# Optimization experiments

Hardware: AMD Instinct MI355X
Metric: run time of the kernel (lower is better)

The kernel has to match this reference:

```python
import jax, jax.numpy as jnp
import numpy as np

N_NODES = 100000
N_EDGES = 3200000
IN_DIM = 128
HID_DIM = 128
N_LAYERS = 3


def setup_inputs() -> dict:
    key = jax.random.key(0)
    ks = jax.random.split(key, 3 + 2 * N_LAYERS)
    inp = {
        "feats": jax.random.normal(ks[0], (N_NODES, IN_DIM), dtype=jnp.float32),
        "edge_src": jax.random.randint(ks[1], (N_EDGES,), 0, N_NODES, dtype=jnp.int32),
        "edge_dst": jax.random.randint(ks[2], (N_EDGES,), 0, N_NODES, dtype=jnp.int32),
    }
    d_in = IN_DIM
    for l in range(N_LAYERS):
        scale = 1.0 / np.sqrt(d_in)
        inp[f"W{l}"] = jax.random.uniform(ks[3 + 2 * l], (d_in, HID_DIM), jnp.float32, -scale, scale)
        inp[f"b{l}"] = jax.random.uniform(ks[4 + 2 * l], (HID_DIM,), jnp.float32, -scale, scale)
        inp[f"eps{l}"] = jnp.zeros((), jnp.float32)  # learn_eps init 0
        d_in = HID_DIM
    return inp


def _gin_layer(h, src, dst, W, b, eps):
    # sum aggregation over in-neighbors: agg[i] = sum_{(s->i)} h[s]
    agg = jax.ops.segment_sum(h[src], dst, num_segments=N_NODES)
    return ((1.0 + eps) * h + agg) @ W + b


def reference(feats, edge_src, edge_dst, W0, b0, eps0, W1, b1, eps1, W2, b2, eps2):
    h = feats
    for W, b, eps in ((W0, b0, eps0), (W1, b1, eps1), (W2, b2, eps2)):
        h = _gin_layer(h, edge_src, edge_dst, W, b, eps)
        # dropout is identity at p=0 / eval
    return h
```

## Files before the change

### kernel.cpp

```cpp
#include <hip/hip_runtime.h>

#define N_NODES 100000
#define N_EDGES 3200000
#define DIM 128
#define GROWS (N_NODES + 1)
#define NBUCK 391
#define NBP 392
#define EB_BLOCKS 782
#define BSLACK 2048
#define MAXPAD 9984

typedef __attribute__((ext_vector_type(8))) short short8;
typedef __attribute__((ext_vector_type(4))) float f32x4;


__device__ __forceinline__ unsigned rne_bf16(float f) {
    unsigned u = __builtin_bit_cast(unsigned, f);
    return (u + 0x7FFFu + ((u >> 16) & 1u)) >> 16;
}
__device__ __forceinline__ float bf16lo(unsigned u) {
    return __builtin_bit_cast(float, u << 16);
}
__device__ __forceinline__ float bf16hi(unsigned u) {
    return __builtin_bit_cast(float, u & 0xFFFF0000u);
}
__device__ __forceinline__ void split2(float x, unsigned short& h, unsigned short& l) {
    unsigned hu = rne_bf16(x);
    h = (unsigned short)hu;
    l = (unsigned short)rne_bf16(x - bf16lo(hu));
}


__global__ __launch_bounds__(256) void bhist_k(const int* __restrict__ dst,
                                               int* __restrict__ bucketTotal,
                                               int* __restrict__ bhArr) {
    __shared__ int h[NBP];
    int tid = threadIdx.x;
    for (int i = tid; i < NBP; i += 256) h[i] = 0;
    __syncthreads();
#pragma unroll
    for (int c = 0; c < 4; c++) {
        int e = blockIdx.x * 4096 + c * 1024 + tid * 4;
        if (e < N_EDGES) {
            int4 d4 = ((const int4*)dst)[e >> 2];
            atomicAdd(&h[d4.x >> 8], 1);
            atomicAdd(&h[d4.y >> 8], 1);
            atomicAdd(&h[d4.z >> 8], 1);
            atomicAdd(&h[d4.w >> 8], 1);
        }
    }
    __syncthreads();
    for (int i = tid; i < NBP; i += 256) {
        int v = h[i];
        bhArr[blockIdx.x * NBP + i] = v;
        if (v > 0) atomicAdd(&bucketTotal[i], v);
    }
}

__global__ __launch_bounds__(512) void bscan_k(const int* __restrict__ bucketTotal,
                                               int* __restrict__ bucketBase,
                                               int* __restrict__ bucketCursor) {
    __shared__ int tmp[512];
    int tid = threadIdx.x;
    int v = (tid < NBP) ? bucketTotal[tid] : 0;
    tmp[tid] = v;
    __syncthreads();
    for (int off = 1; off < 512; off <<= 1) {
        int x = tmp[tid];
        if (tid >= off) x += tmp[tid - off];
        __syncthreads();
        tmp[tid] = x;
        __syncthreads();
    }
    if (tid < NBP) {
        int excl = tmp[tid] - v;
        bucketBase[tid] = excl;
        bucketCursor[tid] = excl;
        if (tid == NBP - 1) bucketBase[NBP] = tmp[tid];
    }
}

__global__ __launch_bounds__(512) void bscatter_k(const int* __restrict__ src,
                                                  const int* __restrict__ dst,
                                                  const int* __restrict__ bhArr,
                                                  int* __restrict__ bucketCursor,
                                                  int* __restrict__ ebuf) {
    __shared__ int lcur0[NBP];
    __shared__ int pexc[NBP];
    __shared__ int lofs[NBP];
    __shared__ int pfx[512];
    __shared__ int sortedv[4096];
    __shared__ int gaddr[4096];
    int tid = threadIdx.x;
    int bid = blockIdx.x;
    int v = 0;
    if (tid < NBP) {
        v = bhArr[bid * NBP + tid];
        lcur0[tid] = (v > 0) ? atomicAdd(&bucketCursor[tid], v) : 0;
    }
    pfx[tid] = v;
    __syncthreads();
    for (int off = 1; off < 512; off <<= 1) {
        int x = pfx[tid];
        if (tid >= off) x += pfx[tid - off];
        __syncthreads();
        pfx[tid] = x;
        __syncthreads();
    }
    if (tid < NBP) {
        int ex = pfx[tid] - v;
        pexc[tid] = ex;
        lofs[tid] = ex;
    }
    __syncthreads();
#pragma unroll
    for (int c = 0; c < 2; c++) {
        int e = bid * 4096 + c * 2048 + tid * 4;
        if (e < N_EDGES) {
            int4 d4 = ((const int4*)dst)[e >> 2];
            int4 s4 = ((const int4*)src)[e >> 2];
            int b0 = d4.x >> 8, b1 = d4.y >> 8, b2 = d4.z >> 8, b3 = d4.w >> 8;
            int t0 = atomicAdd(&lofs[b0], 1);
            int t1 = atomicAdd(&lofs[b1], 1);
            int t2 = atomicAdd(&lofs[b2], 1);
            int t3 = atomicAdd(&lofs[b3], 1);
            sortedv[t0] = (s4.x << 8) | (d4.x & 255);
            sortedv[t1] = (s4.y << 8) | (d4.y & 255);
            sortedv[t2] = (s4.z << 8) | (d4.z & 255);
            sortedv[t3] = (s4.w << 8) | (d4.w & 255);
            gaddr[t0] = lcur0[b0] + (t0 - pexc[b0]);
            gaddr[t1] = lcur0[b1] + (t1 - pexc[b1]);
            gaddr[t2] = lcur0[b2] + (t2 - pexc[b2]);
            gaddr[t3] = lcur0[b3] + (t3 - pexc[b3]);
        }
    }
    __syncthreads();
    int totalE = min(4096, N_EDGES - bid * 4096);
    for (int j = tid; j < totalE; j += 512)
        ebuf[gaddr[j]] = sortedv[j];
}

__global__ __launch_bounds__(256) void bfinal_k(const int* __restrict__ ebuf,
                                                const int* __restrict__ bucketBase,
                                                int* __restrict__ offsets,
                                                int* __restrict__ nbArr,
                                                int* __restrict__ csr) {
    __shared__ int srt[MAXPAD];
    __shared__ int cnt[256];
    __shared__ int sc[256];
    __shared__ int cur[256];
    int tid = threadIdx.x;
    int b = blockIdx.x;
    int s = bucketBase[b], e = bucketBase[b + 1];
    int m = e - s;
    cnt[tid] = 0;
    __syncthreads();
    for (int i = tid; i < m; i += 256)
        atomicAdd(&cnt[ebuf[s + i] & 255], 1);
    __syncthreads();
    int c = cnt[tid];
    int pad = (c + 3) & ~3;
    sc[tid] = pad;
    __syncthreads();
    for (int off = 1; off < 256; off <<= 1) {
        int x = sc[tid];
        if (tid >= off) x += sc[tid - off];
        __syncthreads();
        sc[tid] = x;
        __syncthreads();
    }
    int pexcl = sc[tid] - pad;
    int gbase = s + b * BSLACK;
    int node = b * 256 + tid;
    if (node < N_NODES) {
        offsets[node] = gbase + pexcl;
        nbArr[node] = pad >> 2;
    }
    cur[tid] = pexcl;
    __syncthreads();
    int padTot = sc[255];
    if (padTot <= MAXPAD) {
        for (int j = tid; j < padTot; j += 256) srt[j] = N_NODES;
        __syncthreads();
        for (int i = tid; i < m; i += 256) {
            int pk = ebuf[s + i];
            int pos = atomicAdd(&cur[pk & 255], 1);
            srt[pos] = (int)((unsigned)pk >> 8);
        }
        __syncthreads();
        for (int j = tid; j < padTot; j += 256)
            csr[gbase + j] = srt[j];
    } else {
        for (int i = tid; i < m; i += 256) {
            int pk = ebuf[s + i];
            int pos = atomicAdd(&cur[pk & 255], 1);
            csr[gbase + pos] = (int)((unsigned)pk >> 8);
        }
        __syncthreads();
        int pend = pexcl + pad;
        for (int p2 = cur[tid]; p2 < pend; p2++) csr[gbase + p2] = N_NODES;
    }
}


__global__ __launch_bounds__(64) void prepw_k(const float* __restrict__ W,
                                              unsigned short* __restrict__ Wh,
                                              unsigned short* __restrict__ Wl) {
    int l = threadIdx.x;
    int t = blockIdx.x;
    int col = ((t >> 2) << 4) + (l & 15);
    int k0 = ((t & 3) << 5) + ((l >> 4) << 3);
    unsigned hw[4], lw[4];
#pragma unroll
    for (int p = 0; p < 4; p++) {
        float x0 = W[(size_t)(k0 + 2 * p) * DIM + col];
        float x1 = W[(size_t)(k0 + 2 * p + 1) * DIM + col];
        unsigned short h0, l0, h1, l1;
        split2(x0, h0, l0);
        split2(x1, h1, l1);
        hw[p] = (unsigned)h0 | ((unsigned)h1 << 16);
        lw[p] = (unsigned)l0 | ((unsigned)l1 << 16);
    }
    size_t base = ((size_t)t * 64 + l) * 8;
    *(uint4*)(Wh + base) = make_uint4(hw[0], hw[1], hw[2], hw[3]);
    *(uint4*)(Wl + base) = make_uint4(lw[0], lw[1], lw[2], lw[3]);
}

__global__ __launch_bounds__(256) void gemm_k(const float* __restrict__ H,
                                              const unsigned short* __restrict__ Wh,
                                              const unsigned short* __restrict__ Wl,
                                              unsigned short* __restrict__ G) {
    int tid = threadIdx.x;
    int l = tid & 63;
    int wv = tid >> 6;
    int rowBase = blockIdx.x * 64 + wv * 16;
    int r = rowBase + (l & 15);
    int kg = (l >> 4) << 3;
    const float* hp = H + (size_t)((r < N_NODES) ? r : 0) * DIM;
    float zmask = (r < N_NODES) ? 1.0f : 0.0f;

    f32x4 acc[8];
#pragma unroll
    for (int cb = 0; cb < 8; cb++) acc[cb] = (f32x4){0.f, 0.f, 0.f, 0.f};

#pragma unroll
    for (int ks = 0; ks < 4; ks++) {
        float4 u0 = *(const float4*)(hp + ks * 32 + kg);
        float4 u1 = *(const float4*)(hp + ks * 32 + kg + 4);
        short8 ah, al;
        unsigned short hh, ll;
        split2(u0.x * zmask, hh, ll); ah[0] = hh; al[0] = ll;
        split2(u0.y * zmask, hh, ll); ah[1] = hh; al[1] = ll;
        split2(u0.z * zmask, hh, ll); ah[2] = hh; al[2] = ll;
        split2(u0.w * zmask, hh, ll); ah[3] = hh; al[3] = ll;
        split2(u1.x * zmask, hh, ll); ah[4] = hh; al[4] = ll;
        split2(u1.y * zmask, hh, ll); ah[5] = hh; al[5] = ll;
        split2(u1.z * zmask, hh, ll); ah[6] = hh; al[6] = ll;
        split2(u1.w * zmask, hh, ll); ah[7] = hh; al[7] = ll;
#pragma unroll
        for (int cb = 0; cb < 8; cb++) {
            size_t fidx = (size_t)((cb * 4 + ks) * 64 + l) * 8;
            short8 bh = *(const short8*)(Wh + fidx);
            short8 bl = *(const short8*)(Wl + fidx);
            acc[cb] = __builtin_amdgcn_mfma_f32_16x16x32_bf16(ah, bh, acc[cb], 0, 0, 0);
            acc[cb] = __builtin_amdgcn_mfma_f32_16x16x32_bf16(al, bh, acc[cb], 0, 0, 0);
            acc[cb] = __builtin_amdgcn_mfma_f32_16x16x32_bf16(ah, bl, acc[cb], 0, 0, 0);
        }
    }

    int ro = rowBase + ((l >> 4) << 2);
    int co = l & 15;
#pragma unroll
    for (int cb = 0; cb < 8; cb++) {
#pragma unroll
        for (int j = 0; j < 4; j++) {
            int rr = ro + j;
            if (rr <= N_NODES)
                G[(size_t)rr * DIM + cb * 16 + co] = (unsigned short)rne_bf16(acc[cb][j]);
        }
    }
}

__device__ __forceinline__ void accum8(float* acc, uint4 v) {
    acc[0] += bf16lo(v.x); acc[1] += bf16hi(v.x);
    acc[2] += bf16lo(v.y); acc[3] += bf16hi(v.y);
    acc[4] += bf16lo(v.z); acc[5] += bf16hi(v.z);
    acc[6] += bf16lo(v.w); acc[7] += bf16hi(v.w);
}

__global__ __launch_bounds__(256) void agg_k(const unsigned short* __restrict__ G,
                                             const int* __restrict__ off,
                                             const int* __restrict__ nbArr,
                                             const int* __restrict__ csr,
                                             const float* __restrict__ bias,
                                             const float* __restrict__ epsp,
                                             float* __restrict__ out) {
    int tid = threadIdx.x;
    int lane = tid & 63;
    int node = blockIdx.x * 4 + (tid >> 6);
    int quarter = lane >> 4;
    int q = lane & 15;
    float e1 = 1.0f + epsp[0];

    int offA = off[node];
    int nb = nbArr[node];
    const int* clb = csr + offA + quarter;

    float acc[8] = {0.f, 0.f, 0.f, 0.f, 0.f, 0.f, 0.f, 0.f};

    int b = 0;
    for (; b + 4 <= nb; b += 4) {
        int i0 = clb[0];
        int i1 = clb[4];
        int i2 = clb[8];
        int i3 = clb[12];
        clb += 16;
        uint4 g0 = *(const uint4*)(G + (size_t)i0 * DIM + q * 8);
        uint4 g1 = *(const uint4*)(G + (size_t)i1 * DIM + q * 8);
        uint4 g2 = *(const uint4*)(G + (size_t)i2 * DIM + q * 8);
        uint4 g3 = *(const uint4*)(G + (size_t)i3 * DIM + q * 8);
        accum8(acc, g0);
        accum8(acc, g1);
        accum8(acc, g2);
        accum8(acc, g3);
    }
    for (; b < nb; b++) {
        int i0 = clb[0];
        clb += 4;
        uint4 g0 = *(const uint4*)(G + (size_t)i0 * DIM + q * 8);
        accum8(acc, g0);
    }

#pragma unroll
    for (int j = 0; j < 8; j++) {
        acc[j] += __shfl_xor(acc[j], 16);
        acc[j] += __shfl_xor(acc[j], 32);
    }

    if (quarter == 0) {
        uint4 sv = *(const uint4*)(G + (size_t)node * DIM + q * 8);
        float4 b0 = *(const float4*)(bias + q * 8);
        float4 b1 = *(const float4*)(bias + q * 8 + 4);
        float* op = out + (size_t)node * DIM + q * 8;
        float4 r0, r1;
        r0.x = acc[0] + e1 * bf16lo(sv.x) + b0.x;
        r0.y = acc[1] + e1 * bf16hi(sv.x) + b0.y;
        r0.z = acc[2] + e1 * bf16lo(sv.y) + b0.z;
        r0.w = acc[3] + e1 * bf16hi(sv.y) + b0.w;
        r1.x = acc[4] + e1 * bf16lo(sv.z) + b1.x;
        r1.y = acc[5] + e1 * bf16hi(sv.z) + b1.y;
        r1.z = acc[6] + e1 * bf16lo(sv.w) + b1.z;
        r1.w = acc[7] + e1 * bf16hi(sv.w) + b1.w;
        *(float4*)op = r0;
        *(float4*)(op + 4) = r1;
    }
}


extern "C" void kernel_launch(void* const* d_in, const int* in_sizes, int n_in,
                              void* d_out, int out_size, void* d_ws, size_t ws_size,
                              hipStream_t stream) {
    const float* feats = (const float*)d_in[0];
    const int* esrc = (const int*)d_in[1];
    const int* edst = (const int*)d_in[2];
    const float* Wm[3] = {(const float*)d_in[3], (const float*)d_in[6], (const float*)d_in[9]};
    const float* Bv[3] = {(const float*)d_in[4], (const float*)d_in[7], (const float*)d_in[10]};
    const float* Ev[3] = {(const float*)d_in[5], (const float*)d_in[8], (const float*)d_in[11]};
    float* out = (float*)d_out;

    char* ws = (char*)d_ws;
    unsigned short* bufG = (unsigned short*)(ws);
    int* ebuf       = (int*)(ws + 25600512);
    int* csr        = (int*)(ws + 38400512);
    int* offsets    = (int*)(ws + 54411776);
    int* nbArr      = (int*)(ws + 54811776);
    int* bucketTotal= (int*)(ws + 55211776);
    int* bucketBase = (int*)(ws + 55213376);
    int* bucketCur  = (int*)(ws + 55215040);
    int* bhArr      = (int*)(ws + 55216640);
    unsigned short* wfrag = (unsigned short*)(ws + 56442816);

    for (int l = 0; l < 3; l++)
        prepw_k<<<32, 64, 0, stream>>>(Wm[l], wfrag + l * 32768, wfrag + l * 32768 + 16384);

    hipMemsetAsync(bucketTotal, 0, NBP * sizeof(int), stream);
    bhist_k<<<EB_BLOCKS, 256, 0, stream>>>(edst, bucketTotal, bhArr);
    bscan_k<<<1, 512, 0, stream>>>(bucketTotal, bucketBase, bucketCur);
    bscatter_k<<<EB_BLOCKS, 512, 0, stream>>>(esrc, edst, bhArr, bucketCur, ebuf);
    bfinal_k<<<NBUCK, 256, 0, stream>>>(ebuf, bucketBase, offsets, nbArr, csr);

    const float* h = feats;
    for (int l = 0; l < 3; l++) {
        gemm_k<<<(N_NODES + 63) / 64, 256, 0, stream>>>(h, wfrag + l * 32768,
                                                        wfrag + l * 32768 + 16384, bufG);
        agg_k<<<N_NODES / 4, 256, 0, stream>>>(bufG, offsets, nbArr, csr, Bv[l], Ev[l], out);
        h = out;
    }
}
```

Baseline: 595.6 us.

## Fuse neighbor aggregation with next layer GEMM to keep bf16 intermediates

Adds an aggemm_k kernel. It aggregates neighbor rows for 16 nodes per 1024-thread block, stages the fp32 result in shared memory, then runs the next layer's split-bf16 MFMA GEMM and writes bf16 output directly. It replaces the per-layer gemm_k plus agg_k pair for the first two layers, so the fp32 hidden states are no longer written and re-read through global memory. It also folds the three weight-prep launches into one, ping-pongs intermediates between the workspace and the output buffer, and zeroes the padding row. Only half the waves do the GEMM stage, and the large blocks with a barrier may reduce latency hiding during the gather.

```diff
diff --git a/kernel.cpp b/kernel.cpp
--- a/kernel.cpp
+++ b/kernel.cpp
@@ -203,11 +203,16 @@
 }
 
 
-__global__ __launch_bounds__(64) void prepw_k(const float* __restrict__ W,
-                                              unsigned short* __restrict__ Wh,
-                                              unsigned short* __restrict__ Wl) {
+__global__ __launch_bounds__(64) void prepw_k(const float* __restrict__ W0,
+                                              const float* __restrict__ W1,
+                                              const float* __restrict__ W2,
+                                              unsigned short* __restrict__ wfrag) {
     int l = threadIdx.x;
-    int t = blockIdx.x;
+    int lay = blockIdx.x >> 5;
+    int t = blockIdx.x & 31;
+    const float* W = (lay == 0) ? W0 : (lay == 1) ? W1 : W2;
+    unsigned short* Wh = wfrag + lay * 32768;
+    unsigned short* Wl = Wh + 16384;
     int col = ((t >> 2) << 4) + (l & 15);
     int k0 = ((t & 3) << 5) + ((l >> 4) << 3);
     unsigned hw[4], lw[4];
@@ -286,6 +291,106 @@
     acc[2] += bf16lo(v.y); acc[3] += bf16hi(v.y);
     acc[4] += bf16lo(v.z); acc[5] += bf16hi(v.z);
     acc[6] += bf16lo(v.w); acc[7] += bf16hi(v.w);
+}
+
+__global__ __launch_bounds__(1024) void aggemm_k(const unsigned short* __restrict__ G,
+                                                 const int* __restrict__ off,
+                                                 const int* __restrict__ nbArr,
+                                                 const int* __restrict__ csr,
+                                                 const float* __restrict__ bias,
+                                                 const float* __restrict__ epsp,
+                                                 const unsigned short* __restrict__ Wh,
+                                                 const unsigned short* __restrict__ Wl,
+                                                 unsigned short* __restrict__ Gout) {
+    __shared__ float hsm[16][132];
+    int tid = threadIdx.x;
+    int lane = tid & 63;
+    int wid = tid >> 6;
+    int node = blockIdx.x * 16 + wid;
+    int quarter = lane >> 4;
+    int q = lane & 15;
+    float e1 = 1.0f + epsp[0];
+
+    int offA = off[node];
+    int nb = nbArr[node];
+    const int* clb = csr + offA + quarter;
+    float acc[8] = {0.f, 0.f, 0.f, 0.f, 0.f, 0.f, 0.f, 0.f};
+    int b = 0;
+    for (; b + 4 <= nb; b += 4) {
+        int i0 = clb[0];
+        int i1 = clb[4];
+        int i2 = clb[8];
+        int i3 = clb[12];
+        clb += 16;
+        uint4 g0 = *(const uint4*)(G + (size_t)i0 * DIM + q * 8);
+        uint4 g1 = *(const uint4*)(G + (size_t)i1 * DIM + q * 8);
+        uint4 g2 = *(const uint4*)(G + (size_t)i2 * DIM + q * 8);
+        uint4 g3 = *(const uint4*)(G + (size_t)i3 * DIM + q * 8);
+        accum8(acc, g0);
+        accum8(acc, g1);
+        accum8(acc, g2);
+        accum8(acc, g3);
+    }
+    for (; b < nb; b++) {
+        int i0 = clb[0];
+        clb += 4;
+        uint4 g0 = *(const uint4*)(G + (size_t)i0 * DIM + q * 8);
+        accum8(acc, g0);
+    }
+#pragma unroll
+    for (int j = 0; j < 8; j++) {
+        acc[j] += __shfl_xor(acc[j], 16);
+        acc[j] += __shfl_xor(acc[j], 32);
+    }
+    if (quarter == 0) {
+        uint4 sv = *(const uint4*)(G + (size_t)node * DIM + q * 8);
+        float4 b0 = *(const float4*)(bias + q * 8);
+        float4 b1 = *(const float4*)(bias + q * 8 + 4);
+        float4 r0, r1;
+        r0.x = acc[0] + e1 * bf16lo(sv.x) + b0.x;
+        r0.y = acc[1] + e1 * bf16hi(sv.x) + b0.y;
+        r0.z = acc[2] + e1 * bf16lo(sv.y) + b0.z;
+        r0.w = acc[3] + e1 * bf16hi(sv.y) + b0.w;
+        r1.x = acc[4] + e1 * bf16lo(sv.z) + b1.x;
+        r1.y = acc[5] + e1 * bf16hi(sv.z) + b1.y;
+        r1.z = acc[6] + e1 * bf16lo(sv.w) + b1.z;
+        r1.w = acc[7] + e1 * bf16hi(sv.w) + b1.w;
+        *(float4*)&hsm[wid][q * 8] = r0;
+        *(float4*)&hsm[wid][q * 8 + 4] = r1;
+    }
+    __syncthreads();
+
+    if (wid < 8) {
+        int cb = wid;
+        int rl = lane & 15;
+        int kg = (lane >> 4) << 3;
+        f32x4 o = (f32x4){0.f, 0.f, 0.f, 0.f};
+#pragma unroll
+        for (int ks = 0; ks < 4; ks++) {
+            const float* ap = &hsm[rl][ks * 32 + kg];
+            short8 ah, al;
+            unsigned short hh, ll;
+#pragma unroll
+            for (int j = 0; j < 8; j++) {
+                split2(ap[j], hh, ll);
+                ah[j] = hh;
+                al[j] = ll;
+            }
+            size_t fidx = (size_t)((cb * 4 + ks) * 64 + lane) * 8;
+            short8 bh = *(const short8*)(Wh + fidx);
+            short8 bl = *(const short8*)(Wl + fidx);
+            o = __builtin_amdgcn_mfma_f32_16x16x32_bf16(ah, bh, o, 0, 0, 0);
+            o = __builtin_amdgcn_mfma_f32_16x16x32_bf16(al, bh, o, 0, 0, 0);
+            o = __builtin_amdgcn_mfma_f32_16x16x32_bf16(ah, bl, o, 0, 0, 0);
+        }
+        int ro = blockIdx.x * 16 + ((lane >> 4) << 2);
+        int co = cb * 16 + rl;
+#pragma unroll
+        for (int j = 0; j < 4; j++)
+            Gout[(size_t)(ro + j) * DIM + co] = (unsigned short)rne_bf16(o[j]);
+    } else if (wid == 8 && blockIdx.x == 0) {
+        ((unsigned*)(Gout + (size_t)N_NODES * DIM))[lane] = 0u;
+    }
 }
 
 __global__ __launch_bounds__(256) void agg_k(const unsigned short* __restrict__ G,
@@ -380,8 +485,10 @@
     int* bhArr      = (int*)(ws + 55216640);
     unsigned short* wfrag = (unsigned short*)(ws + 56442816);
 
-    for (int l = 0; l < 3; l++)
-        prepw_k<<<32, 64, 0, stream>>>(Wm[l], wfrag + l * 32768, wfrag + l * 32768 + 16384);
+    unsigned short* G_A = bufG;
+    unsigned short* G_B = (unsigned short*)d_out;
+
+    prepw_k<<<96, 64, 0, stream>>>(Wm[0], Wm[1], Wm[2], wfrag);
 
     hipMemsetAsync(bucketTotal, 0, NBP * sizeof(int), stream);
     bhist_k<<<EB_BLOCKS, 256, 0, stream>>>(edst, bucketTotal, bhArr);
@@ -389,11 +496,10 @@
     bscatter_k<<<EB_BLOCKS, 512, 0, stream>>>(esrc, edst, bhArr, bucketCur, ebuf);
     bfinal_k<<<NBUCK, 256, 0, stream>>>(ebuf, bucketBase, offsets, nbArr, csr);
 
-    const float* h = feats;
-    for (int l = 0; l < 3; l++) {
-        gemm_k<<<(N_NODES + 63) / 64, 256, 0, stream>>>(h, wfrag + l * 32768,
-                                                        wfrag + l * 32768 + 16384, bufG);
-        agg_k<<<N_NODES / 4, 256, 0, stream>>>(bufG, offsets, nbArr, csr, Bv[l], Ev[l], out);
-        h = out;
-    }
-}
+    gemm_k<<<(N_NODES + 64) / 64, 256, 0, stream>>>(feats, wfrag, wfrag + 16384, G_A);
+    aggemm_k<<<N_NODES / 16, 1024, 0, stream>>>(G_A, offsets, nbArr, csr, Bv[0], Ev[0],
+                                                wfrag + 32768, wfrag + 49152, G_B);
+    aggemm_k<<<N_NODES / 16, 1024, 0, stream>>>(G_B, offsets, nbArr, csr, Bv[1], Ev[1],
+                                                wfrag + 65536, wfrag + 81920, G_A);
+    agg_k<<<N_NODES / 4, 256, 0, stream>>>(G_A, offsets, nbArr, csr, Bv[2], Ev[2], out);
+}
```

Measured after the change: 563.8 us. 5.4% less time.
